# Kernel tuning notes

Hardware: AMD Instinct MI355X
Metric: run time of the kernel (lower is better)

## Reference

```python
import jax, jax.numpy as jnp
import numpy as np

B, T, N, PREV_DIM, CURR_DIM = 8, 32, 500, 200, 128
HEADS, UNITS, MSG_UNITS = 4, 64, 64


def setup_inputs() -> dict:
    key = jax.random.key(0)
    k = jax.random.split(key, 6)
    prev_features = jax.random.normal(k[0], (B, N, PREV_DIM), jnp.float32)
    curr_hidden = jax.random.normal(k[1], (B, T, N, CURR_DIM), jnp.float32)
    # glorot-ish small params
    W_src = jax.random.normal(k[2], (HEADS, PREV_DIM, UNITS), jnp.float32) * 0.05
    W_dst = jax.random.normal(k[3], (HEADS, PREV_DIM, UNITS), jnp.float32) * 0.05
    a = jax.random.normal(k[4], (HEADS, UNITS, 1), jnp.float32) * 0.1
    W_msg = jax.random.normal(k[5], (HEADS, CURR_DIM, MSG_UNITS), jnp.float32) * 0.05
    return {"prev_features": prev_features, "curr_hidden": curr_hidden,
            "W_src": W_src, "W_dst": W_dst, "a": a, "W_msg": W_msg}


def reference(prev_features, curr_hidden, W_src, W_dst, a, W_msg):
    # prev_features: [B, N, Dp]; curr_hidden: [B, T, N, Dc]
    heads = W_src.shape[0]
    head_outputs = []
    for h in range(heads):  # small fixed loop over heads (as in original)
        h_src = jnp.einsum('bnd,du->bnu', prev_features, W_src[h])  # [B,N,U]
        h_dst = jnp.einsum('bnd,du->bnu', prev_features, W_dst[h])  # [B,N,U]
        # GATv2 additive scoring: lrelu(src_i + dst_j) . a   -> [B,N,N]
        pairwise = jax.nn.leaky_relu(h_src[:, :, None, :] + h_dst[:, None, :, :], 0.2)
        scores = jnp.einsum('bnmu,u->bnm', pairwise, a[h, :, 0])
        attn = jax.nn.softmax(scores, axis=-1)  # [B,N,N]; dropout is identity at inference
        msg = jnp.einsum('btnd,du->btnu', curr_hidden, W_msg[h])  # [B,T,N,Mu]
        # same graph applied at every timestep (tf.repeat + batched matmul)
        h_prime = jnp.einsum('bnm,btmu->btnu', attn, msg)  # [B,T,N,Mu]
        head_outputs.append(h_prime)
    return jnp.mean(jnp.stack(head_outputs, axis=-1), axis=-1)
```

## Files before the change

kernel.cpp:

```cpp
#include <hip/hip_runtime.h>

#define B_ 8
#define T_ 32
#define N_ 500
#define DP 200
#define DC 128
#define H_ 4
#define U_ 64
#define NP 512
#define COLS (T_ * U_)
#define K4 (H_ * NP)

typedef __attribute__((ext_vector_type(8))) short bf16x8;
typedef __attribute__((ext_vector_type(4))) float f32x4;
typedef __attribute__((ext_vector_type(2))) float f32x2;

typedef const __attribute__((address_space(1))) void* gcptr_t;
typedef __attribute__((address_space(3))) void* lptr_t;

__device__ __forceinline__ void async16(const void* g, void* lds) {
    __builtin_amdgcn_global_load_lds((gcptr_t)g, (lptr_t)lds, 16, 0, 0);
}

__device__ __forceinline__ ushort f2bf(float f) {
    unsigned u = __float_as_uint(f);
    unsigned r = (u + 0x7FFFu + ((u >> 16) & 1u)) >> 16;
    return (ushort)r;
}

__device__ __forceinline__ f32x2 pk_add_sv(unsigned long long sp, f32x2 dp) {
    f32x2 t;
    asm("v_pk_add_f32 %0, %1, %2" : "=v"(t) : "s"(sp), "v"(dp));
    return t;
}

__global__ void prep_wT(const float* __restrict__ Wmsg, ushort* __restrict__ WT) {
    int idx = blockIdx.x * 256 + threadIdx.x;
    int h = idx >> 13, u = (idx >> 7) & 63, d = idx & 127;
    WT[idx] = f2bf(0.25f * Wmsg[((size_t)h * DC + d) * U_ + u]);
}

__global__ void __launch_bounds__(512) proj_all(
    const float* __restrict__ prev, const float* __restrict__ Wsrc,
    const float* __restrict__ Wdst, const float* __restrict__ a_all,
    float* __restrict__ hsrc, float* __restrict__ hdst,
    float* __restrict__ qv)
{
    __shared__ float rows[4 * DP];
    const int tid = threadIdx.x;
    const int bn0 = blockIdx.x * 4;
    for (int e = tid; e < 4 * DP; e += 512) rows[e] = prev[(size_t)bn0 * DP + e];
    __syncthreads();
    const int u = tid & 63;
    const int h = (tid >> 6) & 3;
    const int isdst = tid >> 8;
    const float* W = (isdst ? Wdst : Wsrc) + (size_t)h * DP * U_;
    float a0 = 0.f, a1 = 0.f, a2 = 0.f, a3 = 0.f;
#pragma unroll 4
    for (int d = 0; d < DP; ++d) {
        float w = W[d * U_ + u];
        a0 = fmaf(rows[d], w, a0);
        a1 = fmaf(rows[DP + d], w, a1);
        a2 = fmaf(rows[2 * DP + d], w, a2);
        a3 = fmaf(rows[3 * DP + d], w, a3);
    }
    float acc[4] = {a0, a1, a2, a3};
    float* o = isdst ? hdst : hsrc;
#pragma unroll
    for (int r = 0; r < 4; ++r) {
        int bn = bn0 + r, b = bn / N_, n = bn - b * N_;
        o[(((size_t)b * H_ + h) * N_ + n) * U_ + u] = acc[r];
    }
    if (isdst) {
        const int lane = tid & 63;
        const float av = a_all[(size_t)h * U_ + lane];
#pragma unroll
        for (int r = 0; r < 4; ++r) {
            float v = acc[r] * av;
            for (int off = 1; off < 64; off <<= 1) v += __shfl_xor(v, off);
            if (lane == 0) {
                int bn = bn0 + r, b = bn / N_, n = bn - b * N_;
                qv[((size_t)b * H_ + h) * NP + n] = v;
            }
        }
    }
}

__global__ void __launch_bounds__(512) attn_softmax9(
    const float* __restrict__ hsrc, const float* __restrict__ hdst,
    const float* __restrict__ a_all, const float* __restrict__ qv,
    ushort* __restrict__ attnB)
{
    const int i0 = blockIdx.x * 8, b = blockIdx.y, h = blockIdx.z;
    const int tid = threadIdx.x;
    __shared__ float red[8 * 8];
    __shared__ float s_mx[8], s_rs[8];

    const float* ap = a_all + (size_t)h * U_;
    const float* hb = hsrc + (((size_t)b * H_ + h) * N_) * U_;
    const unsigned long long* sr8[8];
#pragma unroll
    for (int r = 0; r < 8; ++r)
        sr8[r] = (const unsigned long long*)
            (hb + (size_t)min(i0 + r, N_ - 1) * U_);

    const int j = tid;
    const bool valid = j < N_;
    const float4* dp =
        (const float4*)&hdst[(((size_t)b * H_ + h) * N_ + (valid ? j : 0)) * U_];
    const float qj = qv[((size_t)b * H_ + h) * NP + j];

    float av[8] = {0.f, 0.f, 0.f, 0.f, 0.f, 0.f, 0.f, 0.f};
#pragma unroll 1
    for (int kc = 0; kc < 8; ++kc) {
        const int o = kc * 8;
        float4 A = dp[kc * 2 + 0];
        float4 Bv = dp[kc * 2 + 1];
        f32x2 dvp[4];
        dvp[0] = (f32x2){A.x, A.y};  dvp[1] = (f32x2){A.z, A.w};
        dvp[2] = (f32x2){Bv.x, Bv.y}; dvp[3] = (f32x2){Bv.z, Bv.w};
#pragma unroll
        for (int p = 0; p < 4; ++p) {
            const float a_lo = ap[o + p * 2];
            const float a_hi = ap[o + p * 2 + 1];
#pragma unroll
            for (int r = 0; r < 8; ++r) {
                f32x2 t = pk_add_sv(sr8[r][kc * 4 + p], dvp[p]);
                av[r] = fmaf(fabsf(t.x), a_lo, av[r]);
                av[r] = fmaf(fabsf(t.y), a_hi, av[r]);
            }
        }
    }
    const float q6 = 0.6f * qj;
    float sc[8];
#pragma unroll
    for (int r = 0; r < 8; ++r)
        sc[r] = valid ? fmaf(0.4f, av[r], q6) : -1e30f;

    const int wave = tid >> 6, lane = tid & 63;
#pragma unroll
    for (int r = 0; r < 8; ++r) {
        float m = sc[r];
        for (int off = 1; off < 64; off <<= 1) m = fmaxf(m, __shfl_xor(m, off));
        if (lane == 0) red[wave * 8 + r] = m;
    }
    __syncthreads();
    if (tid < 8) {
        float mm = red[tid];
        for (int w = 1; w < 8; ++w) mm = fmaxf(mm, red[w * 8 + tid]);
        s_mx[tid] = mm;
    }
    __syncthreads();
    float e[8];
#pragma unroll
    for (int r = 0; r < 8; ++r) {
        e[r] = __expf(sc[r] - s_mx[r]);
        float s = e[r];
        for (int off = 1; off < 64; off <<= 1) s += __shfl_xor(s, off);
        if (lane == 0) red[wave * 8 + r] = s;
    }
    __syncthreads();
    if (tid < 8) {
        float ss = 0.f;
        for (int w = 0; w < 8; ++w) ss += red[w * 8 + tid];
        s_rs[tid] = 1.0f / ss;
    }
    __syncthreads();
#pragma unroll
    for (int r = 0; r < 8; ++r)
        attnB[(((size_t)b * H_ + h) * NP + i0 + r) * NP + j] =
            f2bf(e[r] * s_rs[r]);
}

__global__ void __launch_bounds__(256) msg_all(
    const float* __restrict__ curr, const ushort* __restrict__ WT,
    ushort* __restrict__ msgT)
{
    __shared__ ushort As[128 * 136];
    const int tid = threadIdx.x;
    const int m0 = blockIdx.x * 128, t = blockIdx.y, b = blockIdx.z;

    const float* cbase = curr + (size_t)(b * T_ + t) * N_ * DC;
#pragma unroll
    for (int it = 0; it < 16; ++it) {
        int e = it * 1024 + tid * 4;
        int r = e >> 7, c = e & 127;
        int gm = m0 + r;
        float4 v; v.x = v.y = v.z = v.w = 0.f;
        if (gm < N_) v = *(const float4*)&cbase[(size_t)gm * DC + c];
        ushort4 o;
        o.x = f2bf(v.x); o.y = f2bf(v.y); o.z = f2bf(v.z); o.w = f2bf(v.w);
        *(ushort4*)&As[r * 136 + c] = o;
    }
    __syncthreads();

    const int wave = tid >> 6, lane = tid & 63;
    const int r15 = lane & 15, quad = lane >> 4;
    const int wm = wave >> 1, wu = wave & 1;

    const ushort* wb = WT + (size_t)(wu * 32 + r15) * DC + quad * 8;

#pragma unroll 1
    for (int h = 0; h < H_; ++h) {
        const ushort* wh = wb + (size_t)h * U_ * DC;
        bf16x8 bg[4][2];
#pragma unroll
        for (int ks = 0; ks < 4; ++ks)
#pragma unroll
            for (int g = 0; g < 2; ++g)
                bg[ks][g] = *(const bf16x8*)&wh[(size_t)(g * 16) * DC + ks * 32];

        f32x4 acc[4][2] = {};
#pragma unroll
        for (int ks = 0; ks < 4; ++ks) {
            bf16x8 af[4];
#pragma unroll
            for (int f = 0; f < 4; ++f)
                af[f] = *(const bf16x8*)&As[(wm * 64 + f * 16 + r15) * 136 + ks * 32 + quad * 8];
#pragma unroll
            for (int f = 0; f < 4; ++f)
#pragma unroll
                for (int g = 0; g < 2; ++g)
                    acc[f][g] = __builtin_amdgcn_mfma_f32_16x16x32_bf16(af[f], bg[ks][g], acc[f][g], 0, 0, 0);
        }
#pragma unroll
        for (int f = 0; f < 4; ++f)
#pragma unroll
            for (int g = 0; g < 2; ++g) {
                int m = m0 + wm * 64 + f * 16 + quad * 4;
                int u = wu * 32 + g * 16 + r15;
                int col = t * U_ + u;
                ushort4 o;
                o.x = f2bf(acc[f][g][0]); o.y = f2bf(acc[f][g][1]);
                o.z = f2bf(acc[f][g][2]); o.w = f2bf(acc[f][g][3]);
                *(ushort4*)&msgT[(((size_t)b * H_ + h) * COLS + col) * NP + m] = o;
            }
    }
}

__global__ void __launch_bounds__(256) gemm_big2(
    const ushort* __restrict__ msgT, const ushort* __restrict__ attnB,
    float* __restrict__ out)
{
    __shared__ ushort As[128 * 64];
    __shared__ ushort Bs[128 * 64];
    const int tid = threadIdx.x;
    const int mt = blockIdx.x, nt = blockIdx.y, b = blockIdx.z;

    const int wave = tid >> 6, lane = tid & 63;
    const int r15 = lane & 15, quad = lane >> 4;
    const int wm = wave >> 1, wn = wave & 1;
    const int lrow = lane >> 3, lch = lane & 7;

    f32x4 acc[4][4] = {};
    for (int kk = 0; kk < K4; kk += 64) {
        const int hh = kk >> 9, ko = kk & (NP - 1);
        const ushort* Ab = msgT + (((size_t)b * H_ + hh) * COLS + mt * 128) * NP + ko;
        const ushort* Bb = attnB + (((size_t)b * H_ + hh) * NP + nt * 128) * NP + ko;
#pragma unroll
        for (int l = 0; l < 4; ++l) {
            const int R0 = wave * 32 + l * 8;
            const int row = R0 + lrow;
            const int gch = lch ^ (row & 7);
            async16(Ab + (size_t)row * NP + gch * 8, &As[R0 * 64]);
            async16(Bb + (size_t)row * NP + gch * 8, &Bs[R0 * 64]);
        }
        __syncthreads();
#pragma unroll
        for (int ks = 0; ks < 2; ++ks) {
            bf16x8 af[4], bg[4];
#pragma unroll
            for (int f = 0; f < 4; ++f) {
                int row = wm * 64 + f * 16 + r15;
                int c = (ks * 4 + quad) ^ (row & 7);
                af[f] = *(const bf16x8*)&As[row * 64 + c * 8];
            }
#pragma unroll
            for (int g = 0; g < 4; ++g) {
                int row = wn * 64 + g * 16 + r15;
                int c = (ks * 4 + quad) ^ (row & 7);
                bg[g] = *(const bf16x8*)&Bs[row * 64 + c * 8];
            }
#pragma unroll
            for (int f = 0; f < 4; ++f)
#pragma unroll
                for (int g = 0; g < 4; ++g)
                    acc[f][g] = __builtin_amdgcn_mfma_f32_16x16x32_bf16(af[f], bg[g], acc[f][g], 0, 0, 0);
        }
        __syncthreads();
    }

    const int t = mt * 2 + wm;
#pragma unroll
    for (int f = 0; f < 4; ++f)
#pragma unroll
        for (int g = 0; g < 4; ++g) {
            int u = f * 16 + quad * 4;
            int i = nt * 128 + wn * 64 + g * 16 + r15;
            if (i < N_) {
                float4 v;
                v.x = acc[f][g][0]; v.y = acc[f][g][1];
                v.z = acc[f][g][2]; v.w = acc[f][g][3];
                *(float4*)&out[(((size_t)b * T_ + t) * N_ + i) * U_ + u] = v;
            }
        }
}

__global__ void __launch_bounds__(256) msg_mfma(
    const float* __restrict__ curr, const ushort* __restrict__ WTh,
    ushort* __restrict__ msgT)
{
    __shared__ ushort As[128 * 136];
    __shared__ ushort Bs[64 * 136];
    const int tid = threadIdx.x;
    const int m0 = blockIdx.x * 128, t = blockIdx.y, b = blockIdx.z;

    const float* cbase = curr + (size_t)(b * T_ + t) * N_ * DC;
#pragma unroll
    for (int it = 0; it < 16; ++it) {
        int e = it * 1024 + tid * 4;
        int r = e >> 7, c = e & 127;
        int gm = m0 + r;
        float4 v; v.x = v.y = v.z = v.w = 0.f;
        if (gm < N_) v = *(const float4*)&cbase[(size_t)gm * DC + c];
        ushort4 o;
        o.x = f2bf(v.x); o.y = f2bf(v.y); o.z = f2bf(v.z); o.w = f2bf(v.w);
        *(ushort4*)&As[r * 136 + c] = o;
    }
#pragma unroll
    for (int it = 0; it < 4; ++it) {
        int e = it * 2048 + tid * 8;
        int u = e >> 7, d = e & 127;
        *(uint4*)&Bs[u * 136 + d] = *(const uint4*)&WTh[u * 128 + d];
    }
    __syncthreads();

    const int wave = tid >> 6, lane = tid & 63;
    const int r15 = lane & 15, quad = lane >> 4;
    const int wm = wave >> 1, wu = wave & 1;

    f32x4 acc[4][2] = {};
#pragma unroll
    for (int ks = 0; ks < 4; ++ks) {
        bf16x8 af[4], bg[2];
#pragma unroll
        for (int f = 0; f < 4; ++f)
            af[f] = *(const bf16x8*)&As[(wm * 64 + f * 16 + r15) * 136 + ks * 32 + quad * 8];
#pragma unroll
        for (int g = 0; g < 2; ++g)
            bg[g] = *(const bf16x8*)&Bs[(wu * 32 + g * 16 + r15) * 136 + ks * 32 + quad * 8];
#pragma unroll
        for (int f = 0; f < 4; ++f)
#pragma unroll
            for (int g = 0; g < 2; ++g)
                acc[f][g] = __builtin_amdgcn_mfma_f32_16x16x32_bf16(af[f], bg[g], acc[f][g], 0, 0, 0);
    }
#pragma unroll
    for (int f = 0; f < 4; ++f)
#pragma unroll
        for (int g = 0; g < 2; ++g) {
            int m = m0 + wm * 64 + f * 16 + quad * 4;
            int u = wu * 32 + g * 16 + r15;
            int col = t * U_ + u;
            ushort4 o;
            o.x = f2bf(acc[f][g][0]); o.y = f2bf(acc[f][g][1]);
            o.z = f2bf(acc[f][g][2]); o.w = f2bf(acc[f][g][3]);
            *(ushort4*)&msgT[((size_t)b * COLS + col) * NP + m] = o;
        }
}

__global__ void __launch_bounds__(256) gemm_mfma(
    const ushort* __restrict__ msgT, const ushort* __restrict__ attnB,
    float* __restrict__ out, int h, int init)
{
    __shared__ ushort As[64 * 72];
    __shared__ ushort Bs[64 * 72];
    const int tid = threadIdx.x;
    const int ct = blockIdx.x, it = blockIdx.y, b = blockIdx.z;

    const ushort* Ab = msgT + ((size_t)b * COLS + ct * 64) * NP;
    const ushort* Bb = attnB + (((size_t)b * H_ + h) * NP + it * 64) * NP;

    const int wave = tid >> 6, lane = tid & 63;
    const int r15 = lane & 15, quad = lane >> 4;
    const int wm = wave >> 1, wn = wave & 1;
    const int srow = tid >> 3, scol = (tid & 7) * 8;

    f32x4 acc[2][2] = {};
    for (int kk = 0; kk < NP; kk += 64) {
#pragma unroll
        for (int it2 = 0; it2 < 2; ++it2) {
            int rr = it2 * 32 + srow;
            *(uint4*)&As[rr * 72 + scol] = *(const uint4*)&Ab[(size_t)rr * NP + kk + scol];
            *(uint4*)&Bs[rr * 72 + scol] = *(const uint4*)&Bb[(size_t)rr * NP + kk + scol];
        }
        __syncthreads();
#pragma unroll
        for (int ks = 0; ks < 2; ++ks) {
            bf16x8 af[2], bg[2];
#pragma unroll
            for (int f = 0; f < 2; ++f)
                af[f] = *(const bf16x8*)&As[(wm * 32 + f * 16 + r15) * 72 + ks * 32 + quad * 8];
#pragma unroll
            for (int g = 0; g < 2; ++g)
                bg[g] = *(const bf16x8*)&Bs[(wn * 32 + g * 16 + r15) * 72 + ks * 32 + quad * 8];
#pragma unroll
            for (int f = 0; f < 2; ++f)
#pragma unroll
                for (int g = 0; g < 2; ++g)
                    acc[f][g] = __builtin_amdgcn_mfma_f32_16x16x32_bf16(af[f], bg[g], acc[f][g], 0, 0, 0);
        }
        __syncthreads();
    }

    const int t = ct;
#pragma unroll
    for (int f = 0; f < 2; ++f)
#pragma unroll
        for (int g = 0; g < 2; ++g) {
            int u = wm * 32 + f * 16 + quad * 4;
            int i = it * 64 + wn * 32 + g * 16 + r15;
            if (i < N_) {
                float* op = out + (((size_t)b * T_ + t) * N_ + i) * U_ + u;
                float4 v;
                v.x = acc[f][g][0]; v.y = acc[f][g][1];
                v.z = acc[f][g][2]; v.w = acc[f][g][3];
                if (!init) {
                    float4 old = *(const float4*)op;
                    v.x += old.x; v.y += old.y; v.z += old.z; v.w += old.w;
                }
                *(float4*)op = v;
            }
        }
}

extern "C" void kernel_launch(void* const* d_in, const int* in_sizes, int n_in,
                              void* d_out, int out_size, void* d_ws, size_t ws_size,
                              hipStream_t stream)
{
    const float* prev = (const float*)d_in[0];
    const float* curr = (const float*)d_in[1];
    const float* Wsrc = (const float*)d_in[2];
    const float* Wdst = (const float*)d_in[3];
    const float* avec = (const float*)d_in[4];
    const float* Wmsg = (const float*)d_in[5];
    float* out = (float*)d_out;

    const size_t attnB_b = (size_t)B_ * H_ * NP * NP * 2;
    const size_t msgT4_b = (size_t)B_ * H_ * COLS * NP * 2;
    const size_t msgT1_b = (size_t)B_ * COLS * NP * 2;
    const size_t WT_b    = (size_t)H_ * U_ * DC * 2;
    const size_t hx_b    = (size_t)B_ * H_ * N_ * U_ * 4;
    const size_t qv_b    = (size_t)B_ * H_ * NP * 4;

    const bool fused = ws_size >= attnB_b + msgT4_b + WT_b + 2 * hx_b + qv_b;
    const size_t msg_b = fused ? msgT4_b : msgT1_b;

    ushort* attnB = (ushort*)d_ws;
    ushort* msgT  = (ushort*)((char*)d_ws + attnB_b);
    ushort* WT    = (ushort*)((char*)d_ws + attnB_b + msg_b);
    float*  hsrc  = (float*)((char*)WT + WT_b);
    float*  hdst  = (float*)((char*)hsrc + hx_b);
    float*  qv    = (float*)((char*)hdst + hx_b);

    prep_wT<<<128, 256, 0, stream>>>(Wmsg, WT);
    proj_all<<<1000, 512, 0, stream>>>(prev, Wsrc, Wdst, avec, hsrc, hdst, qv);
    attn_softmax9<<<dim3(64, B_, H_), 512, 0, stream>>>(hsrc, hdst, avec, qv, attnB);

    if (fused) {
        msg_all<<<dim3(4, T_, B_), 256, 0, stream>>>(curr, WT, msgT);
        gemm_big2<<<dim3(16, 4, B_), 256, 0, stream>>>(msgT, attnB, out);
    } else {
        for (int h = 0; h < H_; ++h) {
            msg_mfma<<<dim3(4, T_, B_), 256, 0, stream>>>(
                curr, WT + (size_t)h * U_ * DC, msgT);
            gemm_mfma<<<dim3(32, 8, B_), 256, 0, stream>>>(
                msgT, attnB, out, h, h == 0 ? 1 : 0);
        }
    }
}
```

Baseline: 273.9 us.

## Load message GEMM A-operand directly to registers, drop LDS staging, use 512 threads

The msg_all kernel no longer stages the curr_hidden tile through shared memory with a block-wide barrier. Each wave now loads its own 32 rows straight from global memory into bf16 MFMA fragments, and the block doubles to 512 threads, so each wave covers half as many rows. This removes LDS writes, LDS reads and the syncthreads, and should give more parallelism for latency hiding. In exchange the global loads are strided per lane instead of fully coalesced, and the padding rows are clamped to N-1, which computes duplicate rows for the padded tail region.

```diff
diff --git a/kernel.cpp b/kernel.cpp
--- a/kernel.cpp
+++ b/kernel.cpp
@@ -172,62 +172,60 @@
             f2bf(e[r] * s_rs[r]);
 }
 
-__global__ void __launch_bounds__(256) msg_all(
+__global__ void __launch_bounds__(512) msg_all(
     const float* __restrict__ curr, const ushort* __restrict__ WT,
     ushort* __restrict__ msgT)
 {
-    __shared__ ushort As[128 * 136];
     const int tid = threadIdx.x;
     const int m0 = blockIdx.x * 128, t = blockIdx.y, b = blockIdx.z;
-
-    const float* cbase = curr + (size_t)(b * T_ + t) * N_ * DC;
-#pragma unroll
-    for (int it = 0; it < 16; ++it) {
-        int e = it * 1024 + tid * 4;
-        int r = e >> 7, c = e & 127;
-        int gm = m0 + r;
-        float4 v; v.x = v.y = v.z = v.w = 0.f;
-        if (gm < N_) v = *(const float4*)&cbase[(size_t)gm * DC + c];
-        ushort4 o;
-        o.x = f2bf(v.x); o.y = f2bf(v.y); o.z = f2bf(v.z); o.w = f2bf(v.w);
-        *(ushort4*)&As[r * 136 + c] = o;
-    }
-    __syncthreads();
-
     const int wave = tid >> 6, lane = tid & 63;
     const int r15 = lane & 15, quad = lane >> 4;
-    const int wm = wave >> 1, wu = wave & 1;
-
-    const ushort* wb = WT + (size_t)(wu * 32 + r15) * DC + quad * 8;
+    const int wrow = (wave >> 1) * 32;
+    const int wu = wave & 1;
+
+    const float* cbase = curr + (size_t)(b * T_ + t) * N_ * DC;
+
+    bf16x8 af[2][4];
+#pragma unroll
+    for (int f = 0; f < 2; ++f) {
+        const int gm = min(m0 + wrow + f * 16 + r15, N_ - 1);
+        const float* rp = cbase + (size_t)gm * DC + quad * 8;
+#pragma unroll
+        for (int ks = 0; ks < 4; ++ks) {
+            float4 lo = *(const float4*)&rp[ks * 32];
+            float4 hi = *(const float4*)&rp[ks * 32 + 4];
+            bf16x8 v;
+            v[0] = (short)f2bf(lo.x); v[1] = (short)f2bf(lo.y);
+            v[2] = (short)f2bf(lo.z); v[3] = (short)f2bf(lo.w);
+            v[4] = (short)f2bf(hi.x); v[5] = (short)f2bf(hi.y);
+            v[6] = (short)f2bf(hi.z); v[7] = (short)f2bf(hi.w);
+            af[f][ks] = v;
+        }
+    }
+
+    const ushort* wbase = WT + (size_t)(wu * 32 + r15) * DC + quad * 8;
 
 #pragma unroll 1
     for (int h = 0; h < H_; ++h) {
-        const ushort* wh = wb + (size_t)h * U_ * DC;
-        bf16x8 bg[4][2];
-#pragma unroll
-        for (int ks = 0; ks < 4; ++ks)
+        const ushort* wh = wbase + (size_t)h * U_ * DC;
+        f32x4 acc[2][2] = {};
+#pragma unroll
+        for (int ks = 0; ks < 4; ++ks) {
+            bf16x8 bg[2];
 #pragma unroll
             for (int g = 0; g < 2; ++g)
-                bg[ks][g] = *(const bf16x8*)&wh[(size_t)(g * 16) * DC + ks * 32];
-
-        f32x4 acc[4][2] = {};
-#pragma unroll
-        for (int ks = 0; ks < 4; ++ks) {
-            bf16x8 af[4];
-#pragma unroll
-            for (int f = 0; f < 4; ++f)
-                af[f] = *(const bf16x8*)&As[(wm * 64 + f * 16 + r15) * 136 + ks * 32 + quad * 8];
-#pragma unroll
-            for (int f = 0; f < 4; ++f)
+                bg[g] = *(const bf16x8*)&wh[(size_t)(g * 16) * DC + ks * 32];
+#pragma unroll
+            for (int f = 0; f < 2; ++f)
 #pragma unroll
                 for (int g = 0; g < 2; ++g)
-                    acc[f][g] = __builtin_amdgcn_mfma_f32_16x16x32_bf16(af[f], bg[ks][g], acc[f][g], 0, 0, 0);
-        }
-#pragma unroll
-        for (int f = 0; f < 4; ++f)
+                    acc[f][g] = __builtin_amdgcn_mfma_f32_16x16x32_bf16(af[f][ks], bg[g], acc[f][g], 0, 0, 0);
+        }
+#pragma unroll
+        for (int f = 0; f < 2; ++f)
 #pragma unroll
             for (int g = 0; g < 2; ++g) {
-                int m = m0 + wm * 64 + f * 16 + quad * 4;
+                int m = m0 + wrow + f * 16 + quad * 4;
                 int u = wu * 32 + g * 16 + r15;
                 int col = t * U_ + u;
                 ushort4 o;
@@ -468,7 +466,7 @@
     attn_softmax9<<<dim3(64, B_, H_), 512, 0, stream>>>(hsrc, hdst, avec, qv, attnB);
 
     if (fused) {
-        msg_all<<<dim3(4, T_, B_), 256, 0, stream>>>(curr, WT, msgT);
+        msg_all<<<dim3(4, T_, B_), 512, 0, stream>>>(curr, WT, msgT);
         gemm_big2<<<dim3(16, 4, B_), 256, 0, stream>>>(msgT, attnB, out);
     } else {
         for (int h = 0; h < H_; ++h) {
```

New measurement: 271.5 us. No clear change (-0.9%).

## Fuse message projection into attention GEMM, eliminating msgT intermediate buffer

Applied to the files above, without the earlier changes.

Replaces the separate message projection and large GEMM kernels with one kernel that computes each head's message tile in LDS from curr_hidden and immediately multiplies it by the attention matrix. This removes the write and re-read of the per-head bf16 message intermediate in global memory. In exchange, each node-half block recomputes the message projection, and attention operands are loaded directly from global memory without LDS staging, adding repeated L2 traffic and syncs.

```diff
diff --git a/kernel.cpp b/kernel.cpp
--- a/kernel.cpp
+++ b/kernel.cpp
@@ -9,18 +9,10 @@
 #define U_ 64
 #define NP 512
 #define COLS (T_ * U_)
-#define K4 (H_ * NP)
 
 typedef __attribute__((ext_vector_type(8))) short bf16x8;
 typedef __attribute__((ext_vector_type(4))) float f32x4;
 typedef __attribute__((ext_vector_type(2))) float f32x2;
-
-typedef const __attribute__((address_space(1))) void* gcptr_t;
-typedef __attribute__((address_space(3))) void* lptr_t;
-
-__device__ __forceinline__ void async16(const void* g, void* lds) {
-    __builtin_amdgcn_global_load_lds((gcptr_t)g, (lptr_t)lds, 16, 0, 0);
-}
 
 __device__ __forceinline__ ushort f2bf(float f) {
     unsigned u = __float_as_uint(f);
@@ -33,6 +25,8 @@
     asm("v_pk_add_f32 %0, %1, %2" : "=v"(t) : "s"(sp), "v"(dp));
     return t;
 }
+
+#define MFMA __builtin_amdgcn_mfma_f32_16x16x32_bf16
 
 __global__ void prep_wT(const float* __restrict__ Wmsg, ushort* __restrict__ WT) {
     int idx = blockIdx.x * 256 + threadIdx.x;
@@ -172,11 +166,114 @@
             f2bf(e[r] * s_rs[r]);
 }
 
-__global__ void __launch_bounds__(256) msg_all(
+__global__ void __launch_bounds__(512) fused_mg(
     const float* __restrict__ curr, const ushort* __restrict__ WT,
+    const ushort* __restrict__ attnB, float* __restrict__ out)
+{
+    __shared__ ushort As[128 * 136];
+    __shared__ ushort Ms[2][64 * 128];
+    const int tid = threadIdx.x;
+    const int t = blockIdx.x, nh = blockIdx.y, b = blockIdx.z;
+    const int wave = tid >> 6, lane = tid & 63;
+    const int r15 = lane & 15, quad = lane >> 4;
+    const int wrow = (wave >> 1) * 32;
+    const int wu = wave & 1;
+    const int n0 = nh * 256 + wave * 32;
+
+    const float* cbase = curr + (size_t)(b * T_ + t) * N_ * DC;
+    const ushort* abase = attnB + (((size_t)b * H_) * NP) * NP;
+
+    f32x4 acc[4][2] = {};
+
+#pragma unroll 1
+    for (int mc = 0; mc < 4; ++mc) {
+        if (mc) __syncthreads();
+#pragma unroll
+        for (int it = 0; it < 8; ++it) {
+            int e = it * 2048 + tid * 4;
+            int r = e >> 7, c = e & 127;
+            int gm = mc * 128 + r;
+            float4 v; v.x = v.y = v.z = v.w = 0.f;
+            if (gm < N_) v = *(const float4*)&cbase[(size_t)gm * DC + c];
+            ushort4 o;
+            o.x = f2bf(v.x); o.y = f2bf(v.y); o.z = f2bf(v.z); o.w = f2bf(v.w);
+            *(ushort4*)&As[r * 136 + c] = o;
+        }
+        __syncthreads();
+
+#pragma unroll 1
+        for (int h = 0; h < H_; ++h) {
+            const int p = h & 1;
+            const ushort* wh = WT + (size_t)h * U_ * DC
+                             + (size_t)(wu * 32 + r15) * DC + quad * 8;
+            f32x4 mg[2][2] = {};
+#pragma unroll
+            for (int ks = 0; ks < 4; ++ks) {
+                bf16x8 bg0 = *(const bf16x8*)&wh[ks * 32];
+                bf16x8 bg1 = *(const bf16x8*)&wh[16 * DC + ks * 32];
+                bf16x8 a0 = *(const bf16x8*)&As[(wrow + r15) * 136 + ks * 32 + quad * 8];
+                bf16x8 a1 = *(const bf16x8*)&As[(wrow + 16 + r15) * 136 + ks * 32 + quad * 8];
+                mg[0][0] = MFMA(a0, bg0, mg[0][0], 0, 0, 0);
+                mg[0][1] = MFMA(a0, bg1, mg[0][1], 0, 0, 0);
+                mg[1][0] = MFMA(a1, bg0, mg[1][0], 0, 0, 0);
+                mg[1][1] = MFMA(a1, bg1, mg[1][1], 0, 0, 0);
+            }
+#pragma unroll
+            for (int f = 0; f < 2; ++f)
+#pragma unroll
+                for (int g = 0; g < 2; ++g) {
+                    const int u = wu * 32 + g * 16 + r15;
+                    const int mp = wrow + f * 16 + quad * 4;
+                    const int unit = (mp >> 3) ^ (u & 7);
+                    ushort4 o;
+                    o.x = f2bf(mg[f][g][0]); o.y = f2bf(mg[f][g][1]);
+                    o.z = f2bf(mg[f][g][2]); o.w = f2bf(mg[f][g][3]);
+                    *(ushort4*)&Ms[p][u * 128 + unit * 8 + (quad & 1) * 4] = o;
+                }
+            __syncthreads();
+
+            const ushort* ab = abase + (size_t)h * NP * NP + mc * 128;
+#pragma unroll
+            for (int ks = 0; ks < 4; ++ks) {
+                bf16x8 bat[2];
+#pragma unroll
+                for (int g = 0; g < 2; ++g)
+                    bat[g] = *(const bf16x8*)
+                        &ab[(size_t)(n0 + g * 16 + r15) * NP + ks * 32 + quad * 8];
+#pragma unroll
+                for (int f = 0; f < 4; ++f) {
+                    const int u = f * 16 + r15;
+                    const int unit = (ks * 4 + quad) ^ (u & 7);
+                    bf16x8 am = *(const bf16x8*)&Ms[p][u * 128 + unit * 8];
+#pragma unroll
+                    for (int g = 0; g < 2; ++g)
+                        acc[f][g] = MFMA(am, bat[g], acc[f][g], 0, 0, 0);
+                }
+            }
+        }
+    }
+
+#pragma unroll
+    for (int f = 0; f < 4; ++f)
+#pragma unroll
+        for (int g = 0; g < 2; ++g) {
+            const int n = n0 + g * 16 + r15;
+            if (n < N_) {
+                float4 v;
+                v.x = acc[f][g][0]; v.y = acc[f][g][1];
+                v.z = acc[f][g][2]; v.w = acc[f][g][3];
+                *(float4*)&out[(((size_t)b * T_ + t) * N_ + n) * U_
+                               + f * 16 + quad * 4] = v;
+            }
+        }
+}
+
+__global__ void __launch_bounds__(256) msg_mfma(
+    const float* __restrict__ curr, const ushort* __restrict__ WTh,
     ushort* __restrict__ msgT)
 {
     __shared__ ushort As[128 * 136];
+    __shared__ ushort Bs[64 * 136];
     const int tid = threadIdx.x;
     const int m0 = blockIdx.x * 128, t = blockIdx.y, b = blockIdx.z;
 
@@ -192,141 +289,6 @@
         o.x = f2bf(v.x); o.y = f2bf(v.y); o.z = f2bf(v.z); o.w = f2bf(v.w);
         *(ushort4*)&As[r * 136 + c] = o;
     }
-    __syncthreads();
-
-    const int wave = tid >> 6, lane = tid & 63;
-    const int r15 = lane & 15, quad = lane >> 4;
-    const int wm = wave >> 1, wu = wave & 1;
-
-    const ushort* wb = WT + (size_t)(wu * 32 + r15) * DC + quad * 8;
-
-#pragma unroll 1
-    for (int h = 0; h < H_; ++h) {
-        const ushort* wh = wb + (size_t)h * U_ * DC;
-        bf16x8 bg[4][2];
-#pragma unroll
-        for (int ks = 0; ks < 4; ++ks)
-#pragma unroll
-            for (int g = 0; g < 2; ++g)
-                bg[ks][g] = *(const bf16x8*)&wh[(size_t)(g * 16) * DC + ks * 32];
-
-        f32x4 acc[4][2] = {};
-#pragma unroll
-        for (int ks = 0; ks < 4; ++ks) {
-            bf16x8 af[4];
-#pragma unroll
-            for (int f = 0; f < 4; ++f)
-                af[f] = *(const bf16x8*)&As[(wm * 64 + f * 16 + r15) * 136 + ks * 32 + quad * 8];
-#pragma unroll
-            for (int f = 0; f < 4; ++f)
-#pragma unroll
-                for (int g = 0; g < 2; ++g)
-                    acc[f][g] = __builtin_amdgcn_mfma_f32_16x16x32_bf16(af[f], bg[ks][g], acc[f][g], 0, 0, 0);
-        }
-#pragma unroll
-        for (int f = 0; f < 4; ++f)
-#pragma unroll
-            for (int g = 0; g < 2; ++g) {
-                int m = m0 + wm * 64 + f * 16 + quad * 4;
-                int u = wu * 32 + g * 16 + r15;
-                int col = t * U_ + u;
-                ushort4 o;
-                o.x = f2bf(acc[f][g][0]); o.y = f2bf(acc[f][g][1]);
-                o.z = f2bf(acc[f][g][2]); o.w = f2bf(acc[f][g][3]);
-                *(ushort4*)&msgT[(((size_t)b * H_ + h) * COLS + col) * NP + m] = o;
-            }
-    }
-}
-
-__global__ void __launch_bounds__(256) gemm_big2(
-    const ushort* __restrict__ msgT, const ushort* __restrict__ attnB,
-    float* __restrict__ out)
-{
-    __shared__ ushort As[128 * 64];
-    __shared__ ushort Bs[128 * 64];
-    const int tid = threadIdx.x;
-    const int mt = blockIdx.x, nt = blockIdx.y, b = blockIdx.z;
-
-    const int wave = tid >> 6, lane = tid & 63;
-    const int r15 = lane & 15, quad = lane >> 4;
-    const int wm = wave >> 1, wn = wave & 1;
-    const int lrow = lane >> 3, lch = lane & 7;
-
-    f32x4 acc[4][4] = {};
-    for (int kk = 0; kk < K4; kk += 64) {
-        const int hh = kk >> 9, ko = kk & (NP - 1);
-        const ushort* Ab = msgT + (((size_t)b * H_ + hh) * COLS + mt * 128) * NP + ko;
-        const ushort* Bb = attnB + (((size_t)b * H_ + hh) * NP + nt * 128) * NP + ko;
-#pragma unroll
-        for (int l = 0; l < 4; ++l) {
-            const int R0 = wave * 32 + l * 8;
-            const int row = R0 + lrow;
-            const int gch = lch ^ (row & 7);
-            async16(Ab + (size_t)row * NP + gch * 8, &As[R0 * 64]);
-            async16(Bb + (size_t)row * NP + gch * 8, &Bs[R0 * 64]);
-        }
-        __syncthreads();
-#pragma unroll
-        for (int ks = 0; ks < 2; ++ks) {
-            bf16x8 af[4], bg[4];
-#pragma unroll
-            for (int f = 0; f < 4; ++f) {
-                int row = wm * 64 + f * 16 + r15;
-                int c = (ks * 4 + quad) ^ (row & 7);
-                af[f] = *(const bf16x8*)&As[row * 64 + c * 8];
-            }
-#pragma unroll
-            for (int g = 0; g < 4; ++g) {
-                int row = wn * 64 + g * 16 + r15;
-                int c = (ks * 4 + quad) ^ (row & 7);
-                bg[g] = *(const bf16x8*)&Bs[row * 64 + c * 8];
-            }
-#pragma unroll
-            for (int f = 0; f < 4; ++f)
-#pragma unroll
-                for (int g = 0; g < 4; ++g)
-                    acc[f][g] = __builtin_amdgcn_mfma_f32_16x16x32_bf16(af[f], bg[g], acc[f][g], 0, 0, 0);
-        }
-        __syncthreads();
-    }
-
-    const int t = mt * 2 + wm;
-#pragma unroll
-    for (int f = 0; f < 4; ++f)
-#pragma unroll
-        for (int g = 0; g < 4; ++g) {
-            int u = f * 16 + quad * 4;
-            int i = nt * 128 + wn * 64 + g * 16 + r15;
-            if (i < N_) {
-                float4 v;
-                v.x = acc[f][g][0]; v.y = acc[f][g][1];
-                v.z = acc[f][g][2]; v.w = acc[f][g][3];
-                *(float4*)&out[(((size_t)b * T_ + t) * N_ + i) * U_ + u] = v;
-            }
-        }
-}
-
-__global__ void __launch_bounds__(256) msg_mfma(
-    const float* __restrict__ curr, const ushort* __restrict__ WTh,
-    ushort* __restrict__ msgT)
-{
-    __shared__ ushort As[128 * 136];
-    __shared__ ushort Bs[64 * 136];
-    const int tid = threadIdx.x;
-    const int m0 = blockIdx.x * 128, t = blockIdx.y, b = blockIdx.z;
-
-    const float* cbase = curr + (size_t)(b * T_ + t) * N_ * DC;
-#pragma unroll
-    for (int it = 0; it < 16; ++it) {
-        int e = it * 1024 + tid * 4;
-        int r = e >> 7, c = e & 127;
-        int gm = m0 + r;
-        float4 v; v.x = v.y = v.z = v.w = 0.f;
-        if (gm < N_) v = *(const float4*)&cbase[(size_t)gm * DC + c];
-        ushort4 o;
-        o.x = f2bf(v.x); o.y = f2bf(v.y); o.z = f2bf(v.z); o.w = f2bf(v.w);
-        *(ushort4*)&As[r * 136 + c] = o;
-    }
 #pragma unroll
     for (int it = 0; it < 4; ++it) {
         int e = it * 2048 + tid * 8;
@@ -353,7 +315,7 @@
         for (int f = 0; f < 4; ++f)
 #pragma unroll
             for (int g = 0; g < 2; ++g)
-                acc[f][g] = __builtin_amdgcn_mfma_f32_16x16x32_bf16(af[f], bg[g], acc[f][g], 0, 0, 0);
+                acc[f][g] = MFMA(af[f], bg[g], acc[f][g], 0, 0, 0);
     }
 #pragma unroll
     for (int f = 0; f < 4; ++f)
@@ -408,7 +370,7 @@
             for (int f = 0; f < 2; ++f)
 #pragma unroll
                 for (int g = 0; g < 2; ++g)
-                    acc[f][g] = __builtin_amdgcn_mfma_f32_16x16x32_bf16(af[f], bg[g], acc[f][g], 0, 0, 0);
+                    acc[f][g] = MFMA(af[f], bg[g], acc[f][g], 0, 0, 0);
         }
         __syncthreads();
     }
@@ -447,14 +409,13 @@
     float* out = (float*)d_out;
 
     const size_t attnB_b = (size_t)B_ * H_ * NP * NP * 2;
-    const size_t msgT4_b = (size_t)B_ * H_ * COLS * NP * 2;
     const size_t msgT1_b = (size_t)B_ * COLS * NP * 2;
     const size_t WT_b    = (size_t)H_ * U_ * DC * 2;
     const size_t hx_b    = (size_t)B_ * H_ * N_ * U_ * 4;
     const size_t qv_b    = (size_t)B_ * H_ * NP * 4;
 
-    const bool fused = ws_size >= attnB_b + msgT4_b + WT_b + 2 * hx_b + qv_b;
-    const size_t msg_b = fused ? msgT4_b : msgT1_b;
+    const bool fused = ws_size >= attnB_b + WT_b + 2 * hx_b + qv_b;
+    const size_t msg_b = fused ? 0 : msgT1_b;
 
     ushort* attnB = (ushort*)d_ws;
     ushort* msgT  = (ushort*)((char*)d_ws + attnB_b);
@@ -468,8 +429,7 @@
     attn_softmax9<<<dim3(64, B_, H_), 512, 0, stream>>>(hsrc, hdst, avec, qv, attnB);
 
     if (fused) {
-        msg_all<<<dim3(4, T_, B_), 256, 0, stream>>>(curr, WT, msgT);
-        gemm_big2<<<dim3(16, 4, B_), 256, 0, stream>>>(msgT, attnB, out);
+        fused_mg<<<dim3(T_, 2, B_), 512, 0, stream>>>(curr, WT, attnB, out);
     } else {
         for (int h = 0; h < H_; ++h) {
             msg_mfma<<<dim3(4, T_, B_), 256, 0, stream>>>(
```

New measurement: 296.0 us. +8.0%, slower.
